# Kernel tuning notes

Hardware: AMD Instinct MI355X
Metric: run time of the kernel (lower is better)

The kernel has to match this reference:

```python
import jax, jax.numpy as jnp
import numpy as np

B = 32
C = 768
NH = 12
HD = C // NH
P = 16
IMG = 224
G = IMG // P           # 14 patches per side
NP = G * G             # 196 patches
DEPTH = 12
PRUNE = [1, 1, 1, 1, 0.5, 0.5, 0.5, 0.5, 0.5, 0.5, 0.5, 0.5]
MOM = 0.5              # momentum for global class-attention update
TRADE = 0.5            # slow-fast tradeoff for placeholder token update
SCALE = HD ** -0.5
NCLS = 1000

def _ln(x, g, b, eps=1e-6):
    mu = jnp.mean(x, -1, keepdims=True)
    var = jnp.mean((x - mu) ** 2, -1, keepdims=True)
    return (x - mu) * jax.lax.rsqrt(var + eps) * g + b

def setup_inputs():
    key = jax.random.key(0)
    ks = iter(jax.random.split(key, 40))
    def rn(shape, s=0.02):
        return jax.random.normal(next(ks), shape, jnp.float32) * s
    return {
        'x_img': jax.random.normal(next(ks), (B, 3, IMG, IMG), jnp.float32),
        'cls_token': rn((1, 1, C)),
        'pos_embed': rn((1, NP + 1, C)),
        'patch_w': rn((3 * P * P, C)),
        'patch_b': rn((C,)),
        'ln1_g': jnp.ones((DEPTH, C), jnp.float32),
        'ln1_b': jnp.zeros((DEPTH, C), jnp.float32),
        'qk_w': rn((DEPTH, C, 2 * C)),
        'qk_b': rn((DEPTH, 2 * C)),
        'v_w': rn((DEPTH, C, C)),
        'v_b': rn((DEPTH, C)),
        'proj_w': rn((DEPTH, C, C)),
        'proj_b': rn((DEPTH, C)),
        'ln2_g': jnp.ones((DEPTH, C), jnp.float32),
        'ln2_b': jnp.zeros((DEPTH, C), jnp.float32),
        'fc1_w': rn((DEPTH, C, 4 * C)),
        'fc1_b': rn((DEPTH, 4 * C)),
        'fc2_w': rn((DEPTH, 4 * C, C)),
        'fc2_b': rn((DEPTH, C)),
        'norm_g': jnp.ones((C,), jnp.float32),
        'norm_b': jnp.zeros((C,), jnp.float32),
        'head_w': rn((C, NCLS)),
        'head_b': rn((NCLS,)),
    }

def reference(x_img, cls_token, pos_embed, patch_w, patch_b, ln1_g, ln1_b,
              qk_w, qk_b, v_w, v_b, proj_w, proj_b, ln2_g, ln2_b,
              fc1_w, fc1_b, fc2_w, fc2_b, norm_g, norm_b, head_w, head_b):
    Bq = x_img.shape[0]
    # PatchEmbed: Conv2d(k=P, stride=P) == flatten each patch as (c, ph, pw) then matmul
    patches = x_img.reshape(Bq, 3, G, P, G, P).transpose(0, 2, 4, 1, 3, 5)
    patches = patches.reshape(Bq, NP, 3 * P * P)
    x = patches @ patch_w + patch_b                                   # [B,196,C]
    x = jnp.concatenate([jnp.broadcast_to(cls_token, (Bq, 1, C)), x], 1)
    x = x + pos_embed                                                 # [B,197,C]

    def block(xt, i):
        # QKAttention + VAttention + proj residual, then MlpBlock residual.
        t = _ln(xt, ln1_g[i], ln1_b[i])
        Nt = t.shape[1]
        qk = (t @ qk_w[i] + qk_b[i]).reshape(Bq, Nt, 2, NH, HD)
        q = qk[:, :, 0].transpose(0, 2, 1, 3)                         # [B,H,Nt,hd]
        k = qk[:, :, 1].transpose(0, 2, 1, 3)
        attn = jax.nn.softmax(jnp.einsum('bhnd,bhmd->bhnm', q, k) * SCALE, -1)
        v = (t @ v_w[i] + v_b[i]).reshape(Bq, Nt, NH, HD).transpose(0, 2, 1, 3)
        o = jnp.einsum('bhnm,bhmd->bhnd', attn, v).transpose(0, 2, 1, 3).reshape(Bq, Nt, C)
        xt = xt + (o @ proj_w[i] + proj_b[i])
        h = _ln(xt, ln2_g[i], ln2_b[i])
        xt = xt + (jax.nn.gelu(h @ fc1_w[i] + fc1_b[i], approximate=False) @ fc2_w[i] + fc2_b[i])
        row = attn[:, :, 0, 1:].sum(1)   # cls-attention row, summed over heads
        return xt, row

    cls_attn = None
    for i in range(DEPTH):
        if PRUNE[i] == 1:
            x, row = block(x, i)
            cls_attn = row if cls_attn is None else (1 - MOM) * cls_attn + MOM * row
        else:
            N_ = int(NP * PRUNE[i])                        # informative token count
            idx = jnp.argsort(-cls_attn, axis=1)           # sort patches by score (easy_gather)
            xp = jnp.take_along_axis(x[:, 1:], idx[:, :, None], axis=1)
            cls_attn = jnp.take_along_axis(cls_attn, idx, axis=1)
            fast = xp[:, N_:]                              # placeholder (pruned) tokens
            score = cls_attn[:, N_:]
            rep = (fast * score[:, :, None]).sum(1, keepdims=True) \
                  / score.sum(1, keepdims=True)[:, :, None]  # representative token
            xs = jnp.concatenate([x[:, :1], xp[:, :N_], rep], 1)   # [B,N_+2,C]
            xs, row = block(xs, i)
            cls_attn = jnp.concatenate(
                [(1 - MOM) * cls_attn[:, :N_] + MOM * row[:, :N_], cls_attn[:, N_:]], 1)
            fast = fast + TRADE * (xs[:, -1:] - rep)       # fast update via rep residual
            x = jnp.concatenate([xs[:, :N_ + 1], fast], 1)  # back to [B,197,C]

    x = _ln(x, norm_g, norm_b)
    return x[:, 0] @ head_w + head_b                        # [B,1000]
```

## Files before the change

### kernel.cpp

```cpp
#include <hip/hip_runtime.h>
#include <hip/hip_bf16.h>
#include <stdint.h>

#define B_ 32
#define C_ 768
#define NH_ 12
#define HD_ 64
#define NP_ 196
#define NTOK 197
#define NKEEP 98
#define NCLS_ 1000
#define MPAD 6400
#define RS_ (3 * C_)

typedef __bf16 bf16x8 __attribute__((ext_vector_type(8)));
typedef float f32x4 __attribute__((ext_vector_type(4)));

__device__ __forceinline__ float blockReduceSum256(float v) {
    __shared__ float red[4];
    const int lane = threadIdx.x & 63, w = threadIdx.x >> 6;
#pragma unroll
    for (int off = 32; off; off >>= 1) v += __shfl_down(v, off);
    __syncthreads();
    if (lane == 0) red[w] = v;
    __syncthreads();
    return red[0] + red[1] + red[2] + red[3];
}

__device__ __forceinline__ void gload16(void* lds, const void* g) {
    __builtin_amdgcn_global_load_lds(
        (const __attribute__((address_space(1))) void*)g,
        (__attribute__((address_space(3))) void*)lds,
        16, 0, 0);
}

__global__ __launch_bounds__(256) void patchify_kernel(const float* __restrict__ img,
                                                       __hip_bfloat16* __restrict__ patches)
{
    const int bp = blockIdx.x;
    const int b = bp / NP_, p = bp % NP_;
    const int gy = p / 14, gx = p % 14;
    const int tid = threadIdx.x;
#pragma unroll
    for (int j = 0; j < 3; ++j) {
        const int e = tid + j * 256;
        const int c = e >> 8, rem = e & 255, py = rem >> 4, px = rem & 15;
        patches[(size_t)bp * C_ + e] = __float2bfloat16(
            img[(((size_t)b * 3 + c) * 224 + gy * 16 + py) * 224 + gx * 16 + px]);
    }
}

__global__ __launch_bounds__(256) void assemble_x_kernel(const float* __restrict__ pemb,
                                                         const float* __restrict__ cls_tok,
                                                         const float* __restrict__ pos,
                                                         float* __restrict__ x)
{
    const int b = blockIdx.x, t = blockIdx.y, tid = threadIdx.x;
#pragma unroll
    for (int j = 0; j < 3; ++j) {
        const int c = tid + j * 256;
        const float v = (t == 0) ? cls_tok[c] : pemb[((size_t)b * NP_ + (t - 1)) * C_ + c];
        x[((size_t)b * NTOK + t) * C_ + c] = v + pos[(size_t)t * C_ + c];
    }
}

__global__ __launch_bounds__(256) void ln_kernel(const float* __restrict__ x,
                                                 const float* __restrict__ g,
                                                 const float* __restrict__ b,
                                                 __hip_bfloat16* outB, float* outF,
                                                 long long inRowStride, int nRows)
{
    const int row = (blockIdx.x << 2) + (threadIdx.x >> 6);
    const int lane = threadIdx.x & 63;
    if (row >= nRows) return;
    const float* xr = x + (size_t)row * inRowStride;
    float4 v0 = *(const float4*)(xr + (lane << 2));
    float4 v1 = *(const float4*)(xr + 256 + (lane << 2));
    float4 v2 = *(const float4*)(xr + 512 + (lane << 2));
    float s = v0.x + v0.y + v0.z + v0.w + v1.x + v1.y + v1.z + v1.w
            + v2.x + v2.y + v2.z + v2.w;
#pragma unroll
    for (int off = 1; off < 64; off <<= 1) s += __shfl_xor(s, off);
    const float mu = s * (1.f / C_);
    float q = 0.f;
    {
        float d;
        d = v0.x - mu; q += d * d; d = v0.y - mu; q += d * d;
        d = v0.z - mu; q += d * d; d = v0.w - mu; q += d * d;
        d = v1.x - mu; q += d * d; d = v1.y - mu; q += d * d;
        d = v1.z - mu; q += d * d; d = v1.w - mu; q += d * d;
        d = v2.x - mu; q += d * d; d = v2.y - mu; q += d * d;
        d = v2.z - mu; q += d * d; d = v2.w - mu; q += d * d;
    }
#pragma unroll
    for (int off = 1; off < 64; off <<= 1) q += __shfl_xor(q, off);
    const float rs = rsqrtf(q * (1.f / C_) + 1e-6f);
    const float4 vv[3] = {v0, v1, v2};
#pragma unroll
    for (int j = 0; j < 3; ++j) {
        const int cbase = (j << 8) + (lane << 2);
        const float4 gv = *(const float4*)(g + cbase);
        const float4 bv = *(const float4*)(b + cbase);
        float o0 = (vv[j].x - mu) * rs * gv.x + bv.x;
        float o1 = (vv[j].y - mu) * rs * gv.y + bv.y;
        float o2 = (vv[j].z - mu) * rs * gv.z + bv.z;
        float o3 = (vv[j].w - mu) * rs * gv.w + bv.w;
        if (outB) {
            union { unsigned short us[4]; uint2 u; } pk;
            __hip_bfloat16 h;
            h = __float2bfloat16(o0); pk.us[0] = *(unsigned short*)&h;
            h = __float2bfloat16(o1); pk.us[1] = *(unsigned short*)&h;
            h = __float2bfloat16(o2); pk.us[2] = *(unsigned short*)&h;
            h = __float2bfloat16(o3); pk.us[3] = *(unsigned short*)&h;
            *(uint2*)((unsigned short*)outB + (size_t)row * C_ + cbase) = pk.u;
        }
        if (outF) {
            float4 o; o.x = o0; o.y = o1; o.z = o2; o.w = o3;
            *(float4*)(outF + (size_t)row * C_ + cbase) = o;
        }
    }
}

__global__ __launch_bounds__(256) void transpose_bf16_kernel(const float* __restrict__ W,
                                                             __hip_bfloat16* __restrict__ Wt,
                                                             int K, int N,
                                                             long long outLstride, long long outOff)
{
    __shared__ float tile[32][33];
    const size_t loffIn = (size_t)blockIdx.z * K * N;
    const size_t loffOut = (size_t)blockIdx.z * outLstride + outOff;
    const int k0 = blockIdx.y << 5, n0 = blockIdx.x << 5;
    const int tid = threadIdx.x;
#pragma unroll
    for (int e = tid; e < 1024; e += 256) {
        const int r = e >> 5, c = e & 31;
        tile[r][c] = W[loffIn + (size_t)(k0 + r) * N + n0 + c];
    }
    __syncthreads();
#pragma unroll
    for (int e = tid; e < 1024; e += 256) {
        const int r = e >> 5, c = e & 31;
        Wt[loffOut + (size_t)(n0 + r) * K + k0 + c] = __float2bfloat16(tile[c][r]);
    }
}

__global__ __launch_bounds__(256) void concat_bias_kernel(const float* __restrict__ qk_b,
                                                          const float* __restrict__ v_b,
                                                          float* __restrict__ out)
{
    const int i = blockIdx.x * 256 + threadIdx.x;
    if (i < 12 * RS_) {
        const int l = i / RS_, c = i % RS_;
        out[i] = (c < 2 * C_) ? qk_b[l * 2 * C_ + c] : v_b[l * C_ + (c - 2 * C_)];
    }
}

template<int GELU, int OMODE>
__global__ __launch_bounds__(256, 4) void gemm_bf16_kernel(const __hip_bfloat16* __restrict__ A,
                                                           const __hip_bfloat16* __restrict__ Bt,
                                                           const float* __restrict__ bias,
                                                           const float* __restrict__ res,
                                                           float* __restrict__ outF,
                                                           __hip_bfloat16* __restrict__ outB,
                                                           int K, int N)
{
    __shared__ __align__(16) unsigned short sMem[16384];
    const int tid = threadIdx.x;
    const int wv = tid >> 6, ln = tid & 63;

    const int nwg = gridDim.x * gridDim.y;
    int lid = blockIdx.y * gridDim.x + blockIdx.x;
    {
        const int q = nwg >> 3, r = nwg & 7;
        const int xcd = lid & 7, lq = lid >> 3;
        lid = (xcd < r ? xcd * (q + 1) : r * (q + 1) + (xcd - r) * q) + lq;
    }
    const int bn = (lid % gridDim.x) << 7;
    const int bm = (lid / gridDim.x) << 7;

    const int wr = wv >> 1, wc = wv & 1;
    const int ln15 = ln & 15, lhi = ln >> 4;

    int offA[2], offB[2];
#pragma unroll
    for (int i = 0; i < 2; ++i) {
        const int s = (i << 8) + tid;
        const int L = s >> 3, cp = (s & 7) ^ (L & 7);
        offA[i] = (bm + (L << 1) + (cp >> 2)) * K + ((cp & 3) << 3);
        offB[i] = (bn + (L << 1) + (cp >> 2)) * K + ((cp & 3) << 3);
    }

    const unsigned ldsBase =
        (unsigned)(size_t)(__attribute__((address_space(3))) unsigned short*)&sMem[0];
    unsigned aOff[4], bOff[4];
#pragma unroll
    for (int m = 0; m < 4; ++m) {
        const int r = (wr << 6) + (m << 4) + ln15;
        const int L = r >> 1;
        const int pc = (((r & 1) << 2) + lhi) ^ (L & 7);
        aOff[m] = (unsigned)((L << 7) + (pc << 4));
    }
#pragma unroll
    for (int n = 0; n < 4; ++n) {
        const int r = (wc << 6) + (n << 4) + ln15;
        const int L = r >> 1;
        const int pc = (((r & 1) << 2) + lhi) ^ (L & 7);
        bOff[n] = (unsigned)(8192 + (L << 7) + (pc << 4));
    }

    f32x4 acc[4][4] = {};

    auto stage = [&](int bufByte, int kt) {
        const int k0 = kt << 5;
        unsigned short* base = sMem + (bufByte >> 1);
        gload16(base + ((0 * 256 + (wv << 6)) << 3), A + offA[0] + k0);
        gload16(base + ((1 * 256 + (wv << 6)) << 3), A + offA[1] + k0);
        gload16(base + 4096 + ((0 * 256 + (wv << 6)) << 3), Bt + offB[0] + k0);
        gload16(base + 4096 + ((1 * 256 + (wv << 6)) << 3), Bt + offB[1] + k0);
    };
    auto compute = [&](unsigned bufOff) {
        bf16x8 a[4], b[4];
#pragma unroll
        for (int m = 0; m < 4; ++m)
            asm volatile("ds_read_b128 %0, %1" : "=v"(a[m]) : "v"(ldsBase + bufOff + aOff[m]));
#pragma unroll
        for (int n = 0; n < 4; ++n)
            asm volatile("ds_read_b128 %0, %1" : "=v"(b[n]) : "v"(ldsBase + bufOff + bOff[n]));
        asm volatile("s_waitcnt lgkmcnt(0)" ::: "memory");
        __builtin_amdgcn_sched_barrier(0);
#pragma unroll
        for (int m = 0; m < 4; ++m)
#pragma unroll
            for (int n = 0; n < 4; ++n)
                acc[m][n] = __builtin_amdgcn_mfma_f32_16x16x32_bf16(a[m], b[n], acc[m][n], 0, 0, 0);
    };

    const int ntiles = K >> 5;
    stage(0, 0);
    asm volatile("s_waitcnt vmcnt(0)" ::: "memory");
    __builtin_amdgcn_s_barrier();
    int t = 0;
    for (; t + 2 < ntiles; t += 2) {
        stage(16384, t + 1);
        asm volatile("s_waitcnt vmcnt(4)" ::: "memory");
        __builtin_amdgcn_s_barrier();
        compute(0u);
        __builtin_amdgcn_s_barrier();
        stage(0, t + 2);
        asm volatile("s_waitcnt vmcnt(4)" ::: "memory");
        __builtin_amdgcn_s_barrier();
        compute(16384u);
        __builtin_amdgcn_s_barrier();
    }
    stage(16384, ntiles - 1);
    asm volatile("s_waitcnt vmcnt(4)" ::: "memory");
    __builtin_amdgcn_s_barrier();
    compute(0u);
    __builtin_amdgcn_s_barrier();
    asm volatile("s_waitcnt vmcnt(0)" ::: "memory");
    __builtin_amdgcn_s_barrier();
    compute(16384u);
    __syncthreads();

    if (OMODE == 0) {
        unsigned short* sOut = sMem;
#pragma unroll
        for (int n = 0; n < 4; ++n) {
            const int col = (wc << 6) + (n << 4) + ln15;
            const float bv = bias[bn + col];
#pragma unroll
            for (int m = 0; m < 4; ++m) {
                const int row0 = (wr << 6) + (m << 4) + (lhi << 2);
#pragma unroll
                for (int r = 0; r < 4; ++r) {
                    float x = acc[m][n][r] + bv;
                    if (GELU) x = 0.5f * x * (1.f + erff(x * 0.70710678118654752f));
                    const __hip_bfloat16 hb = __float2bfloat16(x);
                    sOut[(row0 + r) * 128 + col] = *(const unsigned short*)&hb;
                }
            }
        }
        __syncthreads();
#pragma unroll
        for (int i = 0; i < 8; ++i) {
            const int chunk = (i << 8) + tid;
            const int row = chunk >> 4, c8 = (chunk & 15) << 3;
            *(uint4*)((unsigned short*)outB + (size_t)(bm + row) * N + bn + c8) =
                *(const uint4*)(sOut + row * 128 + c8);
        }
    } else {
#pragma unroll
        for (int n = 0; n < 4; ++n) {
            const int gcn = bn + (wc << 6) + (n << 4) + ln15;
            const float bv = bias[gcn];
#pragma unroll
            for (int m = 0; m < 4; ++m) {
                const int gr0 = bm + (wr << 6) + (m << 4) + (lhi << 2);
                f32x4 v = acc[m][n];
#pragma unroll
                for (int r = 0; r < 4; ++r) {
                    const size_t o = (size_t)(gr0 + r) * N + gcn;
                    float x = v[r] + bv;
                    if (OMODE == 1) x += res[o];
                    outF[o] = x;
                }
            }
        }
    }
}

template<int OMODE>
__global__ __launch_bounds__(256, 4) void gemm_half_kernel(const __hip_bfloat16* __restrict__ A,
                                                           const __hip_bfloat16* __restrict__ Bt,
                                                           const float* __restrict__ bias,
                                                           const float* __restrict__ res,
                                                           float* __restrict__ outF,
                                                           int K, int N)
{
    __shared__ __align__(16) unsigned short sMem[2 * 6144];
    const int tid = threadIdx.x;
    const int wv = tid >> 6, ln = tid & 63;

    const int nwg = gridDim.x * gridDim.y;
    int lid = blockIdx.y * gridDim.x + blockIdx.x;
    {
        const int q = nwg >> 3, r = nwg & 7;
        const int xcd = lid & 7, lq = lid >> 3;
        lid = (xcd < r ? xcd * (q + 1) : r * (q + 1) + (xcd - r) * q) + lq;
    }
    const int bn = (lid % gridDim.x) << 7;
    const int bm = (lid / gridDim.x) << 6;

    const int wr = wv >> 1, wc = wv & 1;
    const int ln15 = ln & 15, lhi = ln >> 4;

    int offA, offB[2];
    {
        const int L = tid >> 3, cp = (tid & 7) ^ (L & 7);
        offA = (bm + (L << 1) + (cp >> 2)) * K + ((cp & 3) << 3);
    }
#pragma unroll
    for (int i = 0; i < 2; ++i) {
        const int s = (i << 8) + tid;
        const int L = s >> 3, cp = (s & 7) ^ (L & 7);
        offB[i] = (bn + (L << 1) + (cp >> 2)) * K + ((cp & 3) << 3);
    }

    const unsigned ldsBase =
        (unsigned)(size_t)(__attribute__((address_space(3))) unsigned short*)&sMem[0];
    unsigned aOff[2], bOff[4];
#pragma unroll
    for (int m = 0; m < 2; ++m) {
        const int r = (wr << 5) + (m << 4) + ln15;
        const int L = r >> 1;
        const int pc = (((r & 1) << 2) + lhi) ^ (L & 7);
        aOff[m] = (unsigned)((L << 7) + (pc << 4));
    }
#pragma unroll
    for (int n = 0; n < 4; ++n) {
        const int r = (wc << 6) + (n << 4) + ln15;
        const int L = r >> 1;
        const int pc = (((r & 1) << 2) + lhi) ^ (L & 7);
        bOff[n] = (unsigned)(4096 + (L << 7) + (pc << 4));
    }

    f32x4 acc[2][4] = {};

    auto stage = [&](int bufUShort, int kt) {
        const int k0 = kt << 5;
        unsigned short* base = sMem + bufUShort;
        gload16(base + ((wv << 6) << 3), A + offA + k0);
        gload16(base + 2048 + ((0 * 256 + (wv << 6)) << 3), Bt + offB[0] + k0);
        gload16(base + 2048 + ((1 * 256 + (wv << 6)) << 3), Bt + offB[1] + k0);
    };
    auto compute = [&](unsigned bufByte) {
        bf16x8 a[2], b[4];
#pragma unroll
        for (int m = 0; m < 2; ++m)
            asm volatile("ds_read_b128 %0, %1" : "=v"(a[m]) : "v"(ldsBase + bufByte + aOff[m]));
#pragma unroll
        for (int n = 0; n < 4; ++n)
            asm volatile("ds_read_b128 %0, %1" : "=v"(b[n]) : "v"(ldsBase + bufByte + bOff[n]));
        asm volatile("s_waitcnt lgkmcnt(0)" ::: "memory");
        __builtin_amdgcn_sched_barrier(0);
#pragma unroll
        for (int m = 0; m < 2; ++m)
#pragma unroll
            for (int n = 0; n < 4; ++n)
                acc[m][n] = __builtin_amdgcn_mfma_f32_16x16x32_bf16(a[m], b[n], acc[m][n], 0, 0, 0);
    };

    const int ntiles = K >> 5;
    stage(0, 0);
    asm volatile("s_waitcnt vmcnt(0)" ::: "memory");
    __builtin_amdgcn_s_barrier();
    int t = 0;
    for (; t + 2 < ntiles; t += 2) {
        stage(6144, t + 1);
        asm volatile("s_waitcnt vmcnt(3)" ::: "memory");
        __builtin_amdgcn_s_barrier();
        compute(0u);
        __builtin_amdgcn_s_barrier();
        stage(0, t + 2);
        asm volatile("s_waitcnt vmcnt(3)" ::: "memory");
        __builtin_amdgcn_s_barrier();
        compute(12288u);
        __builtin_amdgcn_s_barrier();
    }
    stage(6144, ntiles - 1);
    asm volatile("s_waitcnt vmcnt(3)" ::: "memory");
    __builtin_amdgcn_s_barrier();
    compute(0u);
    __builtin_amdgcn_s_barrier();
    asm volatile("s_waitcnt vmcnt(0)" ::: "memory");
    __builtin_amdgcn_s_barrier();
    compute(12288u);

#pragma unroll
    for (int n = 0; n < 4; ++n) {
        const int gcn = bn + (wc << 6) + (n << 4) + ln15;
        const float bv = bias[gcn];
#pragma unroll
        for (int m = 0; m < 2; ++m) {
            const int gr0 = bm + (wr << 5) + (m << 4) + (lhi << 2);
            f32x4 v = acc[m][n];
#pragma unroll
            for (int r = 0; r < 4; ++r) {
                const size_t o = (size_t)(gr0 + r) * N + gcn;
                float x = v[r] + bv;
                if (OMODE == 1) x += res[o];
                outF[o] = x;
            }
        }
    }
}

__global__ __launch_bounds__(256) void head_kernel(const float* __restrict__ A,
                                                   const float* __restrict__ W,
                                                   const float* __restrict__ bias,
                                                   float* __restrict__ out)
{
    const int n = blockIdx.x * 256 + threadIdx.x;
    const int m = blockIdx.y;
    if (n >= NCLS_) return;
    const float* a = A + (size_t)m * C_;
    float s = 0.f;
#pragma unroll 8
    for (int k = 0; k < C_; ++k) s = fmaf(a[k], W[(size_t)k * NCLS_ + n], s);
    out[(size_t)m * NCLS_ + n] = s + bias[n];
}

template<int NT16>
__global__ __launch_bounds__(256) void attn_mfma_kernel(const __hip_bfloat16* __restrict__ qkv,
                                                        __hip_bfloat16* __restrict__ o,
                                                        float* __restrict__ attn0,
                                                        int Nt)
{
    constexpr int NPAD = NT16 * 16;
    constexpr int PSW = (((NPAD / 8) & 7) == 0) ? 7 : 3;
    constexpr int VSW = 7;
    constexpr int PROWB = NPAD * 2 + 16;
    constexpr int VROWB = (NPAD == 224) ? 528 : 272;
    __shared__ unsigned short sK[NPAD * 64 + 512];
    __shared__ unsigned short sV[32 * VROWB];

    const int bh = blockIdx.x;
    const int b = bh / NH_, h = bh % NH_;
    const int qtile = blockIdx.y;
    const int tid = threadIdx.x, ln = tid & 63, wv = tid >> 6;
    const int ln15 = ln & 15, lhi = ln >> 4;
    const __hip_bfloat16* qkbase = qkv + (size_t)b * Nt * RS_;

#pragma unroll
    for (int it = 0; it < NPAD * 8 / 256; ++it) {
        const int p = it * 256 + tid;
        int key = p >> 3;
        const int c = (p & 7) ^ (key & 7);
        if (key >= Nt) key = Nt - 1;
        unsigned short* dst = sK + (size_t)(it * 256 + (wv << 6)) * 8;
        gload16(dst, qkbase + (size_t)key * RS_ + C_ + (h << 6) + (c << 3));
    }
#pragma unroll
    for (int it = 0; it < NPAD * 8 / 256; ++it) {
        const int e = it * 256 + tid;
        const int key = e >> 3, dc = e & 7;
        union { uint4 u; unsigned short us[8]; } val;
        val.u = make_uint4(0u, 0u, 0u, 0u);
        if (key < Nt)
            val.u = *(const uint4*)(qkbase + (size_t)key * RS_ + 2 * C_ + (h << 6) + (dc << 3));
        const int kc = key >> 3, kb = (key & 7) << 1;
#pragma unroll
        for (int j = 0; j < 8; ++j) {
            const int d = (dc << 3) + j;
            *(unsigned short*)((char*)sV + d * VROWB + ((kc ^ ((d >> 3) & VSW)) << 4) + kb) = val.us[j];
        }
    }
    const int qbase = qtile * 64 + (wv << 4);
    int qrow = qbase + ln15; if (qrow >= Nt) qrow = Nt - 1;
    const __hip_bfloat16* qp = qkbase + (size_t)qrow * RS_ + (h << 6) + (lhi << 3);
    const bf16x8 qf0 = *(const bf16x8*)qp;
    const bf16x8 qf1 = *(const bf16x8*)(qp + 32);
    __syncthreads();

    f32x4 sc[NT16];
#pragma unroll
    for (int t = 0; t < NT16; ++t) {
        const int key = (t << 4) + ln15;
        const unsigned short* kr = sK + (size_t)key * 64;
        const bf16x8 k0 = *(const bf16x8*)(kr + ((lhi ^ (key & 7)) << 3));
        const bf16x8 k1 = *(const bf16x8*)(kr + (((4 + lhi) ^ (key & 7)) << 3));
        f32x4 a = {0.f, 0.f, 0.f, 0.f};
        a = __builtin_amdgcn_mfma_f32_16x16x32_bf16(k0, qf0, a, 0, 0, 0);
        a = __builtin_amdgcn_mfma_f32_16x16x32_bf16(k1, qf1, a, 0, 0, 0);
        sc[t] = a;
    }
    __syncthreads();

    float mx = -1e30f;
#pragma unroll
    for (int t = 0; t < NT16; ++t)
#pragma unroll
        for (int r = 0; r < 4; ++r) {
            const int key = (t << 4) + (lhi << 2) + r;
            const float v = (key < Nt) ? sc[t][r] * 0.125f : -1e30f;
            sc[t][r] = v;
            mx = fmaxf(mx, v);
        }
    mx = fmaxf(mx, __shfl_xor(mx, 16));
    mx = fmaxf(mx, __shfl_xor(mx, 32));
    float sum = 0.f;
#pragma unroll
    for (int t = 0; t < NT16; ++t)
#pragma unroll
        for (int r = 0; r < 4; ++r) {
            const float e = expf(sc[t][r] - mx);
            sc[t][r] = e; sum += e;
        }
    sum += __shfl_xor(sum, 16);
    sum += __shfl_xor(sum, 32);
    const float inv = 1.f / sum;

    char* Pw = (char*)sK + wv * (16 * PROWB);
    const bool isQ0 = (qtile == 0) && (wv == 0) && (ln15 == 0);
#pragma unroll
    for (int t = 0; t < NT16; ++t) {
        union { unsigned short us[4]; uint2 u2; } pk;
#pragma unroll
        for (int r = 0; r < 4; ++r) {
            const float p = sc[t][r] * inv;
            const __hip_bfloat16 hb = __float2bfloat16(p);
            pk.us[r] = *(const unsigned short*)&hb;
            if (isQ0) {
                const int key = (t << 4) + (lhi << 2) + r;
                if (key < Nt) attn0[(size_t)bh * NTOK + key] = p;
            }
        }
        const int chunk = ((t << 1) + (lhi >> 1)) ^ (ln15 & PSW);
        *(uint2*)(Pw + ln15 * PROWB + (chunk << 4) + ((lhi & 1) << 3)) = pk.u2;
    }
    __syncthreads();

    f32x4 oa[4] = {};
#pragma unroll
    for (int s = 0; s < NPAD / 32; ++s) {
        const bf16x8 pf = *(const bf16x8*)(Pw + ln15 * PROWB +
                                           ((((s << 2) + lhi) ^ (ln15 & PSW)) << 4));
#pragma unroll
        for (int n = 0; n < 4; ++n) {
            const int d = (n << 4) + ln15;
            const bf16x8 vf = *(const bf16x8*)((char*)sV + d * VROWB +
                                               ((((s << 2) + lhi) ^ ((d >> 3) & VSW)) << 4));
            oa[n] = __builtin_amdgcn_mfma_f32_16x16x32_bf16(pf, vf, oa[n], 0, 0, 0);
        }
    }
#pragma unroll
    for (int n = 0; n < 4; ++n)
#pragma unroll
        for (int r = 0; r < 4; ++r) {
            const int qq = qbase + (lhi << 2) + r;
            if (qq < Nt)
                o[((size_t)b * Nt + qq) * C_ + (h << 6) + (n << 4) + ln15] =
                    __float2bfloat16(oa[n][r]);
        }
}

__global__ __launch_bounds__(256) void row_cls_ema_kernel(const float* __restrict__ attn0,
                                                          float* __restrict__ cls, int first)
{
    const int b = blockIdx.x, t = threadIdx.x;
    if (t < NP_) {
        float s = 0.f;
#pragma unroll
        for (int h = 0; h < NH_; ++h) s += attn0[((size_t)(b * NH_ + h)) * NTOK + 1 + t];
        const int i = b * NP_ + t;
        cls[i] = first ? s : 0.5f * cls[i] + 0.5f * s;
    }
}

__global__ __launch_bounds__(256) void row_cls_prune_kernel(const float* __restrict__ attn0,
                                                            const float* __restrict__ sorted,
                                                            float* __restrict__ cls)
{
    const int b = blockIdx.x, t = threadIdx.x;
    if (t < NP_) {
        float sv = sorted[b * NP_ + t];
        if (t < NKEEP) {
            float s = 0.f;
#pragma unroll
            for (int h = 0; h < NH_; ++h) s += attn0[((size_t)(b * NH_ + h)) * NTOK + 1 + t];
            sv = 0.5f * sv + 0.5f * s;
        }
        cls[b * NP_ + t] = sv;
    }
}

__global__ __launch_bounds__(256) void rank_kernel(const float* __restrict__ cls,
                                                   int* __restrict__ idx,
                                                   float* __restrict__ sorted,
                                                   float* __restrict__ ssum)
{
    __shared__ float sv[NP_];
    const int b = blockIdx.x, t = threadIdx.x;
    if (t < NP_) sv[t] = cls[b * NP_ + t];
    __syncthreads();
    float val = 0.f; int r = NP_;
    if (t < NP_) {
        val = sv[t];
        r = 0;
        for (int j = 0; j < NP_; ++j) {
            const float vj = sv[j];
            r += (vj > val || (vj == val && j < t)) ? 1 : 0;
        }
        idx[b * NP_ + r] = t;
        sorted[b * NP_ + r] = val;
    }
    const float contrib = (t < NP_ && r >= NKEEP) ? val : 0.f;
    const float tot = blockReduceSum256(contrib);
    if (t == 0) ssum[b] = tot;
}

__global__ __launch_bounds__(256) void build_xs_kernel(const float* __restrict__ x,
                                                       const int* __restrict__ idx,
                                                       const float* __restrict__ sorted,
                                                       const float* __restrict__ ssum,
                                                       float* __restrict__ xs,
                                                       float* __restrict__ fast,
                                                       float* __restrict__ rep)
{
    const int b = blockIdx.x, t = blockIdx.y, tid = threadIdx.x;
    const float* xb = x + (size_t)b * NTOK * C_;
    if (t == 0) {
#pragma unroll
        for (int j = 0; j < 3; ++j) {
            const int c = tid + j * 256;
            xs[(size_t)b * 100 * C_ + c] = xb[c];
        }
    } else if (t <= NKEEP) {
        const int src = 1 + idx[b * NP_ + (t - 1)];
#pragma unroll
        for (int j = 0; j < 3; ++j) {
            const int c = tid + j * 256;
            xs[((size_t)b * 100 + t) * C_ + c] = xb[(size_t)src * C_ + c];
        }
    } else if (t == NKEEP + 1) {
        const float inv = 1.f / ssum[b];
        float acc0 = 0.f, acc1 = 0.f, acc2 = 0.f;
        for (int jj = 0; jj < NP_ - NKEEP; ++jj) {
            const int src = 1 + idx[b * NP_ + NKEEP + jj];
            const float wgt = sorted[b * NP_ + NKEEP + jj];
            const float* xr = xb + (size_t)src * C_;
            acc0 = fmaf(xr[tid], wgt, acc0);
            acc1 = fmaf(xr[tid + 256], wgt, acc1);
            acc2 = fmaf(xr[tid + 512], wgt, acc2);
        }
        float* xsr = xs + ((size_t)b * 100 + 99) * C_;
        float* rr = rep + (size_t)b * C_;
        xsr[tid] = acc0 * inv;       rr[tid] = acc0 * inv;
        xsr[tid + 256] = acc1 * inv; rr[tid + 256] = acc1 * inv;
        xsr[tid + 512] = acc2 * inv; rr[tid + 512] = acc2 * inv;
    } else {
        const int jf = t - (NKEEP + 2);
        const int src = 1 + idx[b * NP_ + NKEEP + jf];
#pragma unroll
        for (int j = 0; j < 3; ++j) {
            const int c = tid + j * 256;
            fast[((size_t)b * (NP_ - NKEEP) + jf) * C_ + c] = xb[(size_t)src * C_ + c];
        }
    }
}

__global__ __launch_bounds__(256) void scatter_back_kernel(const float* __restrict__ xs,
                                                           const float* __restrict__ fast,
                                                           const float* __restrict__ rep,
                                                           float* __restrict__ x)
{
    const int b = blockIdx.x, t = blockIdx.y, tid = threadIdx.x;
#pragma unroll
    for (int j = 0; j < 3; ++j) {
        const int c = tid + j * 256;
        float v;
        if (t <= NKEEP)
            v = xs[((size_t)b * 100 + t) * C_ + c];
        else
            v = fast[((size_t)b * (NP_ - NKEEP) + (t - NKEEP - 1)) * C_ + c]
                + 0.5f * (xs[((size_t)b * 100 + 99) * C_ + c] - rep[(size_t)b * C_ + c]);
        x[((size_t)b * NTOK + t) * C_ + c] = v;
    }
}

extern "C" void kernel_launch(void* const* d_in, const int* in_sizes, int n_in,
                              void* d_out, int out_size, void* d_ws, size_t ws_size,
                              hipStream_t stream)
{
    (void)in_sizes; (void)n_in; (void)out_size;
    const float* x_img   = (const float*)d_in[0];
    const float* cls_tok = (const float*)d_in[1];
    const float* pos     = (const float*)d_in[2];
    const float* patch_w = (const float*)d_in[3];
    const float* patch_b = (const float*)d_in[4];
    const float* ln1_g   = (const float*)d_in[5];
    const float* ln1_b   = (const float*)d_in[6];
    const float* qk_w    = (const float*)d_in[7];
    const float* qk_b    = (const float*)d_in[8];
    const float* v_w     = (const float*)d_in[9];
    const float* v_b     = (const float*)d_in[10];
    const float* proj_w  = (const float*)d_in[11];
    const float* proj_b  = (const float*)d_in[12];
    const float* ln2_g   = (const float*)d_in[13];
    const float* ln2_b   = (const float*)d_in[14];
    const float* fc1_w   = (const float*)d_in[15];
    const float* fc1_b   = (const float*)d_in[16];
    const float* fc2_w   = (const float*)d_in[17];
    const float* fc2_b   = (const float*)d_in[18];
    const float* norm_g  = (const float*)d_in[19];
    const float* norm_b  = (const float*)d_in[20];
    const float* head_w  = (const float*)d_in[21];
    const float* head_b  = (const float*)d_in[22];

    char* base = (char*)d_ws;
    size_t off = 0;
    auto alloc = [&](size_t bytes) -> void* {
        void* p = base + off; off = (off + bytes + 255) & ~(size_t)255; return p;
    };
    float* X    = (float*)alloc((size_t)MPAD * C_ * 4);
    __hip_bfloat16* Tb   = (__hip_bfloat16*)alloc((size_t)MPAD * C_ * 2);
    __hip_bfloat16* QKVb = (__hip_bfloat16*)alloc((size_t)MPAD * RS_ * 2);
    __hip_bfloat16* Hb   = (__hip_bfloat16*)alloc((size_t)MPAD * 4 * C_ * 2);
    float* XS   = (float*)alloc((size_t)3200 * C_ * 4);
    float* FAST = (float*)alloc((size_t)B_ * (NP_ - NKEEP) * C_ * 4);
    float* REP  = (float*)alloc((size_t)B_ * C_ * 4);
    float* ATTN0= (float*)alloc((size_t)B_ * NH_ * NTOK * 4);
    float* CLS  = (float*)alloc((size_t)B_ * NP_ * 4);
    float* SORT = (float*)alloc((size_t)B_ * NP_ * 4);
    float* SSUM = (float*)alloc((size_t)B_ * 4);
    float* T0   = (float*)alloc((size_t)B_ * C_ * 4);
    int*   IDX  = (int*)alloc((size_t)B_ * NP_ * 4);
    float* BIASQKV = (float*)alloc((size_t)12 * RS_ * 4);
    __hip_bfloat16* WTpatch = (__hip_bfloat16*)alloc((size_t)C_ * C_ * 2);
    __hip_bfloat16* WTqkv   = (__hip_bfloat16*)alloc((size_t)12 * RS_ * C_ * 2);
    __hip_bfloat16* WTproj  = (__hip_bfloat16*)alloc((size_t)12 * C_ * C_ * 2);
    __hip_bfloat16* WTfc1   = (__hip_bfloat16*)alloc((size_t)12 * C_ * 4 * C_ * 2);
    __hip_bfloat16* WTfc2   = (__hip_bfloat16*)alloc((size_t)12 * 4 * C_ * C_ * 2);
    if (off > ws_size) return;

    __hip_bfloat16* Ob    = Hb;
    __hip_bfloat16* PATCH = Hb;
    float*          PEMB  = (float*)QKVb;

    const dim3 blk(256);

    transpose_bf16_kernel<<<dim3(24, 24, 1), blk, 0, stream>>>(patch_w, WTpatch, C_, C_, (long long)C_ * C_, 0);
    transpose_bf16_kernel<<<dim3(48, 24, 12), blk, 0, stream>>>(qk_w, WTqkv, C_, 2 * C_, (long long)RS_ * C_, 0);
    transpose_bf16_kernel<<<dim3(24, 24, 12), blk, 0, stream>>>(v_w, WTqkv, C_, C_, (long long)RS_ * C_, (long long)2 * C_ * C_);
    transpose_bf16_kernel<<<dim3(24, 24, 12), blk, 0, stream>>>(proj_w, WTproj, C_, C_, (long long)C_ * C_, 0);
    transpose_bf16_kernel<<<dim3(96, 24, 12), blk, 0, stream>>>(fc1_w, WTfc1, C_, 4 * C_, (long long)4 * C_ * C_, 0);
    transpose_bf16_kernel<<<dim3(24, 96, 12), blk, 0, stream>>>(fc2_w, WTfc2, 4 * C_, C_, (long long)4 * C_ * C_, 0);
    concat_bias_kernel<<<(12 * RS_ + 255) / 256, blk, 0, stream>>>(qk_b, v_b, BIASQKV);

    auto runBlock = [&](int i, float* xb, int Nt) {
        const int M = B_ * Nt;
        const int mt = (M + 127) >> 7;
        const int mt64 = (M + 63) >> 6;
        const int qtiles = (Nt + 63) >> 6;
        ln_kernel<<<(M + 3) / 4, blk, 0, stream>>>(xb, ln1_g + i * C_, ln1_b + i * C_, Tb, nullptr, C_, M);
        gemm_bf16_kernel<0, 0><<<dim3(RS_ / 128, mt), blk, 0, stream>>>(
            Tb, WTqkv + (size_t)i * RS_ * C_, BIASQKV + (size_t)i * RS_, nullptr, nullptr, QKVb, C_, RS_);
        if (Nt == NTOK)
            attn_mfma_kernel<14><<<dim3(B_ * NH_, qtiles), blk, 0, stream>>>(QKVb, Ob, ATTN0, Nt);
        else
            attn_mfma_kernel<8><<<dim3(B_ * NH_, qtiles), blk, 0, stream>>>(QKVb, Ob, ATTN0, Nt);
        gemm_half_kernel<1><<<dim3(6, mt64), blk, 0, stream>>>(
            Ob, WTproj + (size_t)i * C_ * C_, proj_b + (size_t)i * C_, xb, xb, C_, C_);
        ln_kernel<<<(M + 3) / 4, blk, 0, stream>>>(xb, ln2_g + i * C_, ln2_b + i * C_, Tb, nullptr, C_, M);
        gemm_bf16_kernel<1, 0><<<dim3(24, mt), blk, 0, stream>>>(
            Tb, WTfc1 + (size_t)i * C_ * 4 * C_, fc1_b + (size_t)i * 4 * C_, nullptr, nullptr, Hb, C_, 4 * C_);
        gemm_half_kernel<1><<<dim3(6, mt64), blk, 0, stream>>>(
            Hb, WTfc2 + (size_t)i * 4 * C_ * C_, fc2_b + (size_t)i * C_, xb, xb, 4 * C_, C_);
    };

    patchify_kernel<<<B_ * NP_, blk, 0, stream>>>(x_img, PATCH);
    gemm_half_kernel<2><<<dim3(6, 98), blk, 0, stream>>>(
        PATCH, WTpatch, patch_b, nullptr, PEMB, C_, C_);
    assemble_x_kernel<<<dim3(B_, NTOK), blk, 0, stream>>>(PEMB, cls_tok, pos, X);

    for (int i = 0; i < 12; ++i) {
        if (i < 4) {
            runBlock(i, X, NTOK);
            row_cls_ema_kernel<<<B_, blk, 0, stream>>>(ATTN0, CLS, i == 0 ? 1 : 0);
        } else {
            rank_kernel<<<B_, blk, 0, stream>>>(CLS, IDX, SORT, SSUM);
            build_xs_kernel<<<dim3(B_, 198), blk, 0, stream>>>(X, IDX, SORT, SSUM, XS, FAST, REP);
            runBlock(i, XS, 100);
            scatter_back_kernel<<<dim3(B_, NTOK), blk, 0, stream>>>(XS, FAST, REP, X);
            row_cls_prune_kernel<<<B_, blk, 0, stream>>>(ATTN0, SORT, CLS);
        }
    }

    ln_kernel<<<8, blk, 0, stream>>>(X, norm_g, norm_b, nullptr, T0, (long long)NTOK * C_, B_);
    head_kernel<<<dim3(4, B_), blk, 0, stream>>>(T0, head_w, head_b, (float*)d_out);
}
```

Baseline: 2.489 ms.

## Triple-buffer half-tile GEMM pipeline and fuse LN1 into pruned-token gather

The 64x128 GEMM used for proj, fc2 and patch embedding moves from a 2-stage to a 3-stage LDS ring. This keeps two K-tiles of global loads in flight and is meant to hide memory latency better, at the cost of more shared memory per block and lower occupancy. Separately, build_xs now computes layernorm-1 on each gathered row and writes the bf16 normalized rows directly, so the separate ln_kernel launch for the pruned blocks is skipped. The fused version adds two block reductions inside the gather kernel and assumes K/32 is at least 3 in the pipeline tail.

```diff
diff --git a/kernel.cpp b/kernel.cpp
--- a/kernel.cpp
+++ b/kernel.cpp
@@ -317,7 +317,7 @@
                                                            float* __restrict__ outF,
                                                            int K, int N)
 {
-    __shared__ __align__(16) unsigned short sMem[2 * 6144];
+    __shared__ __align__(16) unsigned short sMem[3 * 6144];
     const int tid = threadIdx.x;
     const int wv = tid >> 6, ln = tid & 63;
 
@@ -392,29 +392,37 @@
 
     const int ntiles = K >> 5;
     stage(0, 0);
-    asm volatile("s_waitcnt vmcnt(0)" ::: "memory");
-    __builtin_amdgcn_s_barrier();
+    stage(6144, 1);
     int t = 0;
-    for (; t + 2 < ntiles; t += 2) {
-        stage(6144, t + 1);
-        asm volatile("s_waitcnt vmcnt(3)" ::: "memory");
+    for (; t + 6 <= ntiles; t += 3) {
+        stage(12288, t + 2);
+        asm volatile("s_waitcnt vmcnt(6)" ::: "memory");
         __builtin_amdgcn_s_barrier();
         compute(0u);
         __builtin_amdgcn_s_barrier();
-        stage(0, t + 2);
-        asm volatile("s_waitcnt vmcnt(3)" ::: "memory");
+        stage(0, t + 3);
+        asm volatile("s_waitcnt vmcnt(6)" ::: "memory");
         __builtin_amdgcn_s_barrier();
         compute(12288u);
         __builtin_amdgcn_s_barrier();
-    }
-    stage(6144, ntiles - 1);
-    asm volatile("s_waitcnt vmcnt(3)" ::: "memory");
+        stage(6144, t + 4);
+        asm volatile("s_waitcnt vmcnt(6)" ::: "memory");
+        __builtin_amdgcn_s_barrier();
+        compute(24576u);
+        __builtin_amdgcn_s_barrier();
+    }
+    stage(12288, ntiles - 1);
+    asm volatile("s_waitcnt vmcnt(6)" ::: "memory");
     __builtin_amdgcn_s_barrier();
     compute(0u);
     __builtin_amdgcn_s_barrier();
+    asm volatile("s_waitcnt vmcnt(3)" ::: "memory");
+    __builtin_amdgcn_s_barrier();
+    compute(12288u);
+    __builtin_amdgcn_s_barrier();
     asm volatile("s_waitcnt vmcnt(0)" ::: "memory");
     __builtin_amdgcn_s_barrier();
-    compute(12288u);
+    compute(24576u);
 
 #pragma unroll
     for (int n = 0; n < 4; ++n) {
@@ -645,39 +653,41 @@
                                                        const float* __restrict__ ssum,
                                                        float* __restrict__ xs,
                                                        float* __restrict__ fast,
-                                                       float* __restrict__ rep)
+                                                       float* __restrict__ rep,
+                                                       const float* __restrict__ lng,
+                                                       const float* __restrict__ lnb,
+                                                       __hip_bfloat16* __restrict__ tb)
 {
     const int b = blockIdx.x, t = blockIdx.y, tid = threadIdx.x;
     const float* xb = x + (size_t)b * NTOK * C_;
+
+    float v0, v1, v2;
+    int ldsRow = -1;
+
     if (t == 0) {
-#pragma unroll
-        for (int j = 0; j < 3; ++j) {
-            const int c = tid + j * 256;
-            xs[(size_t)b * 100 * C_ + c] = xb[c];
-        }
+        v0 = xb[tid]; v1 = xb[tid + 256]; v2 = xb[tid + 512];
+        ldsRow = 0;
     } else if (t <= NKEEP) {
         const int src = 1 + idx[b * NP_ + (t - 1)];
-#pragma unroll
-        for (int j = 0; j < 3; ++j) {
-            const int c = tid + j * 256;
-            xs[((size_t)b * 100 + t) * C_ + c] = xb[(size_t)src * C_ + c];
-        }
+        const float* xr = xb + (size_t)src * C_;
+        v0 = xr[tid]; v1 = xr[tid + 256]; v2 = xr[tid + 512];
+        ldsRow = t;
     } else if (t == NKEEP + 1) {
         const float inv = 1.f / ssum[b];
-        float acc0 = 0.f, acc1 = 0.f, acc2 = 0.f;
+        float a0 = 0.f, a1 = 0.f, a2 = 0.f;
         for (int jj = 0; jj < NP_ - NKEEP; ++jj) {
             const int src = 1 + idx[b * NP_ + NKEEP + jj];
             const float wgt = sorted[b * NP_ + NKEEP + jj];
             const float* xr = xb + (size_t)src * C_;
-            acc0 = fmaf(xr[tid], wgt, acc0);
-            acc1 = fmaf(xr[tid + 256], wgt, acc1);
-            acc2 = fmaf(xr[tid + 512], wgt, acc2);
-        }
-        float* xsr = xs + ((size_t)b * 100 + 99) * C_;
-        float* rr = rep + (size_t)b * C_;
-        xsr[tid] = acc0 * inv;       rr[tid] = acc0 * inv;
-        xsr[tid + 256] = acc1 * inv; rr[tid + 256] = acc1 * inv;
-        xsr[tid + 512] = acc2 * inv; rr[tid + 512] = acc2 * inv;
+            a0 = fmaf(xr[tid], wgt, a0);
+            a1 = fmaf(xr[tid + 256], wgt, a1);
+            a2 = fmaf(xr[tid + 512], wgt, a2);
+        }
+        v0 = a0 * inv; v1 = a1 * inv; v2 = a2 * inv;
+        rep[(size_t)b * C_ + tid] = v0;
+        rep[(size_t)b * C_ + tid + 256] = v1;
+        rep[(size_t)b * C_ + tid + 512] = v2;
+        ldsRow = 99;
     } else {
         const int jf = t - (NKEEP + 2);
         const int src = 1 + idx[b * NP_ + NKEEP + jf];
@@ -686,7 +696,20 @@
             const int c = tid + j * 256;
             fast[((size_t)b * (NP_ - NKEEP) + jf) * C_ + c] = xb[(size_t)src * C_ + c];
         }
-    }
+        return;
+    }
+
+    float* xsr = xs + ((size_t)b * 100 + ldsRow) * C_;
+    xsr[tid] = v0; xsr[tid + 256] = v1; xsr[tid + 512] = v2;
+
+    const float mu = blockReduceSum256(v0 + v1 + v2) * (1.f / C_);
+    const float d0 = v0 - mu, d1 = v1 - mu, d2 = v2 - mu;
+    const float var = blockReduceSum256(d0 * d0 + d1 * d1 + d2 * d2) * (1.f / C_);
+    const float rs = rsqrtf(var + 1e-6f);
+    __hip_bfloat16* tr = tb + ((size_t)b * 100 + ldsRow) * C_;
+    tr[tid]       = __float2bfloat16(d0 * rs * lng[tid]       + lnb[tid]);
+    tr[tid + 256] = __float2bfloat16(d1 * rs * lng[tid + 256] + lnb[tid + 256]);
+    tr[tid + 512] = __float2bfloat16(d2 * rs * lng[tid + 512] + lnb[tid + 512]);
 }
 
 __global__ __launch_bounds__(256) void scatter_back_kernel(const float* __restrict__ xs,
@@ -777,12 +800,13 @@
     transpose_bf16_kernel<<<dim3(24, 96, 12), blk, 0, stream>>>(fc2_w, WTfc2, 4 * C_, C_, (long long)4 * C_ * C_, 0);
     concat_bias_kernel<<<(12 * RS_ + 255) / 256, blk, 0, stream>>>(qk_b, v_b, BIASQKV);
 
-    auto runBlock = [&](int i, float* xb, int Nt) {
+    auto runBlock = [&](int i, float* xb, int Nt, bool skipLn1) {
         const int M = B_ * Nt;
         const int mt = (M + 127) >> 7;
         const int mt64 = (M + 63) >> 6;
         const int qtiles = (Nt + 63) >> 6;
-        ln_kernel<<<(M + 3) / 4, blk, 0, stream>>>(xb, ln1_g + i * C_, ln1_b + i * C_, Tb, nullptr, C_, M);
+        if (!skipLn1)
+            ln_kernel<<<(M + 3) / 4, blk, 0, stream>>>(xb, ln1_g + i * C_, ln1_b + i * C_, Tb, nullptr, C_, M);
         gemm_bf16_kernel<0, 0><<<dim3(RS_ / 128, mt), blk, 0, stream>>>(
             Tb, WTqkv + (size_t)i * RS_ * C_, BIASQKV + (size_t)i * RS_, nullptr, nullptr, QKVb, C_, RS_);
         if (Nt == NTOK)
@@ -805,12 +829,13 @@
 
     for (int i = 0; i < 12; ++i) {
         if (i < 4) {
-            runBlock(i, X, NTOK);
+            runBlock(i, X, NTOK, false);
             row_cls_ema_kernel<<<B_, blk, 0, stream>>>(ATTN0, CLS, i == 0 ? 1 : 0);
         } else {
             rank_kernel<<<B_, blk, 0, stream>>>(CLS, IDX, SORT, SSUM);
-            build_xs_kernel<<<dim3(B_, 198), blk, 0, stream>>>(X, IDX, SORT, SSUM, XS, FAST, REP);
-            runBlock(i, XS, 100);
+            build_xs_kernel<<<dim3(B_, 198), blk, 0, stream>>>(
+                X, IDX, SORT, SSUM, XS, FAST, REP, ln1_g + i * C_, ln1_b + i * C_, Tb);
+            runBlock(i, XS, 100, true);
             scatter_back_kernel<<<dim3(B_, NTOK), blk, 0, stream>>>(XS, FAST, REP, X);
             row_cls_prune_kernel<<<B_, blk, 0, stream>>>(ATTN0, SORT, CLS);
         }
```

Result: no change. 2.478 ms (-0.4%).
